# Optimization experiments

Measured on AMD Instinct MI355X. Metric: run time of the kernel, lower is better.

Reference implementation:

```python
import jax, jax.numpy as jnp
import numpy as np

B, N, D, K = 32, 4096, 128, 512
NPB = 2048          # unique tail nodes per batch (>= K so topk branch is taken)
M = B * NPB         # total unique tail nodes
E = B * N           # total edges
NUM_ENT = 10000


def setup_inputs() -> dict:
    key = jax.random.key(0)
    ks = jax.random.split(key, 18)
    f = lambda k, s: jax.random.normal(k, s, dtype=jnp.float32)
    inp = {
        "q_head": f(ks[0], (B, D)),
        "q_rel": f(ks[1], (B, D)),
        "q_time": f(ks[2], (B, D)),
        "r_neighbor": f(ks[3], (B, N, D)),
        "t_neighbor": f(ks[4], (B, N, D)),
        "time_neighbor": f(ks[5], (B, N, D)),
        "hidden": f(ks[6], (E, D)),
        "tail_emd": jnp.zeros((M, D), jnp.float32),  # scatter out-buffer
    }
    # tail_index: each edge of batch b scatters into that batch's node slab
    local = jax.random.randint(ks[7], (B, N), 0, NPB)
    inp["tail_index"] = (local + jnp.arange(B)[:, None] * NPB).reshape(E).astype(jnp.int32)
    # tail_nodes: [M,3] = (batch id, tail entity, time)
    batch_col = jnp.repeat(jnp.arange(B), NPB)
    tail_col = jax.random.randint(ks[8], (M,), 0, NUM_ENT)
    time_col = jax.random.randint(ks[9], (M,), 0, 365)
    inp["tail_nodes"] = jnp.stack([batch_col, tail_col, time_col], axis=-1).astype(jnp.int32)
    # linear-layer params (torch nn.Linear-style scaling)
    s3, s1 = 1.0 / np.sqrt(3 * D), 1.0 / np.sqrt(D)
    inp["W_q"] = f(ks[10], (3 * D, D)) * s3
    inp["b_q"] = jnp.zeros((D,), jnp.float32)
    inp["W_a"] = f(ks[11], (3 * D, D)) * s3
    inp["b_a"] = jnp.zeros((D,), jnp.float32)
    inp["W_att"] = f(ks[12], (3 * D, 1)) * s3
    inp["b_att"] = jnp.zeros((1,), jnp.float32)
    inp["W_rule"] = f(ks[13], (D, 1)) * s1
    inp["b_rule"] = jnp.zeros((1,), jnp.float32)
    inp["W_out"] = f(ks[14], (D, D)) * s1
    inp["b_out"] = jnp.zeros((D,), jnp.float32)
    return inp


def reference(q_head, q_rel, q_time, r_neighbor, t_neighbor, time_neighbor,
              hidden, tail_emd, tail_index, tail_nodes,
              W_q, b_q, W_a, b_a, W_att, b_att, W_rule, b_rule, W_out, b_out):
    # act = identity (module default). reduce = 'sum'.
    # raw message per edge: [E, D]
    message = (q_head[:, None, :] + r_neighbor + time_neighbor).reshape(E, D)
    # query / neighbor projections
    query = jnp.concatenate([q_head, q_rel, q_time], axis=-1) @ W_q + b_q      # [B, D]
    neigh = jnp.concatenate([r_neighbor, t_neighbor, time_neighbor], -1) @ W_a + b_a  # [B, N, D]
    q = query[:, None, :]
    qa = jnp.concatenate([q * neigh, q - neigh, q + neigh], axis=-1)           # [B, N, 3D]
    att1 = jax.nn.sigmoid(qa @ W_att + b_att).reshape(E, 1)
    att2 = jax.nn.sigmoid(hidden @ W_rule + b_rule)                            # [E, 1]
    att = (att1 + att2) * 0.5
    msg = att * message
    # scatter-sum aggregation over unique tail nodes
    seg = lambda v: jax.ops.segment_sum(v, tail_index, num_segments=M)
    tail_agg = tail_emd + seg(msg)            # scatter(..., out=tail_emd)
    new_hidden = seg(hidden)                  # [M, D]
    agg_att = seg(att[:, 0])                  # [M]
    # per-batch top-k over aggregated attention (each batch has NPB >= K nodes)
    nodes_batch = tail_nodes[:, 0]
    scores = jnp.where(nodes_batch[None, :] == jnp.arange(B)[:, None],
                       agg_att[None, :], -jnp.inf)                             # [B, M]
    _, idx = jax.lax.top_k(scores, K)                                          # [B, K] global node ids
    new_nodes = jnp.stack([tail_nodes[:, 1][idx], tail_nodes[:, 2][idx]], -1)  # [B, K, 2]
    emd = tail_agg[idx]                                                        # [B, K, D]
    hid = new_hidden[idx]                                                      # [B, K, D]
    out_emd = emd @ W_out + b_out                                              # act=identity
    return new_nodes, out_emd, hid
```

## Files before the change

### kernel.cpp

```cpp
#include <hip/hip_runtime.h>
#include <math.h>

#define B 32
#define N 4096
#define D 128
#define KTOP 512
#define NPB 2048
#define MSEG (B * NPB)
#define E (B * N)
#define MAXC 32
#define K7ROWS 16

__global__ __launch_bounds__(384) void k0_precompute(
    const float* __restrict__ qh, const float* __restrict__ qr,
    const float* __restrict__ qt, const float* __restrict__ Wq,
    const float* __restrict__ bq, const float* __restrict__ Wa,
    const float* __restrict__ ba, const float* __restrict__ Watt,
    const float* __restrict__ batt, float* __restrict__ vf,
    float* __restrict__ c2f, int* __restrict__ counts,
    double* __restrict__ aggd) {
  int b = blockIdx.x;
  int tid = threadIdx.x;
  {
    int t = b * 384 + tid;
    float4 z = make_float4(0.f, 0.f, 0.f, 0.f);
    float4* cz = (float4*)counts;
    float4* az = (float4*)aggd;
    for (int i = t; i < 16384; i += 12288) cz[i] = z;
    for (int i = t; i < 32768; i += 12288) az[i] = z;
  }
  int d = tid & 127;
  int g = tid >> 7;
  __shared__ double part[3][128];
  __shared__ double u[128];
  __shared__ double red[128];
  const float* xs = (g == 0 ? qh : (g == 1 ? qr : qt)) + b * 128;
  const float* Wg = Wq + g * 128 * 128;
  double a0 = 0, a1 = 0, a2 = 0, a3 = 0;
#pragma unroll 4
  for (int i = 0; i < 128; i += 4) {
    a0 += (double)xs[i] * (double)Wg[i * 128 + d];
    a1 += (double)xs[i + 1] * (double)Wg[(i + 1) * 128 + d];
    a2 += (double)xs[i + 2] * (double)Wg[(i + 2) * 128 + d];
    a3 += (double)xs[i + 3] * (double)Wg[(i + 3) * 128 + d];
  }
  part[g][d] = (a0 + a1) + (a2 + a3);
  __syncthreads();
  if (g == 0) {
    double acc = (double)bq[d] + part[0][d] + part[1][d] + part[2][d];
    double w1 = (double)Watt[d], w2 = (double)Watt[128 + d],
           w3 = (double)Watt[256 + d];
    double ud = acc * w1 - w2 + w3;
    u[d] = ud;
    red[d] = acc * (w2 + w3) + (double)ba[d] * ud;
  }
  __syncthreads();
  for (int s = 64; s > 0; s >>= 1) {
    if (tid < s) red[tid] += red[tid + s];
    __syncthreads();
  }
  if (tid == 0) c2f[b] = (float)(red[0] + (double)batt[0]);
  {
    double v0 = 0, v1 = 0, v2 = 0, v3 = 0;
    const float* Wr = Wa + tid * 128;
#pragma unroll 4
    for (int dd = 0; dd < 128; dd += 4) {
      v0 += (double)Wr[dd] * u[dd];
      v1 += (double)Wr[dd + 1] * u[dd + 1];
      v2 += (double)Wr[dd + 2] * u[dd + 2];
      v3 += (double)Wr[dd + 3] * u[dd + 3];
    }
    vf[b * 384 + tid] = (float)((v0 + v1) + (v2 + v3));
  }
}

__global__ __launch_bounds__(256, 8) void k1_att(
    const float* __restrict__ r, const float* __restrict__ t,
    const float* __restrict__ tm, const float* __restrict__ hidden,
    const float* __restrict__ Wrule, const float* __restrict__ brule,
    const float* __restrict__ vf, const float* __restrict__ c2f,
    const int* __restrict__ tidx, float* __restrict__ attw,
    double* __restrict__ aggd, int* __restrict__ counts,
    unsigned short* __restrict__ lists) {
  int tid = threadIdx.x;
  int h = tid >> 5;
  int l = tid & 31;
  int blk = blockIdx.x;
  int b = blk >> 5;
  const float4* vb = (const float4*)(vf + b * 384);
  float4 v0 = vb[l];
  float4 v1 = vb[32 + l];
  float4 v2 = vb[64 + l];
  float4 wr = ((const float4*)Wrule)[l];
  float c2 = c2f[b];
  float br = brule[0];
  unsigned lo = (unsigned)(l * 4);
  for (int pass = 0; pass < 2; ++pass) {
    int base = blk * 128 + pass * 64;
    int myseg = 0;
    if (l < 8) myseg = tidx[base + l * 8 + h];
    float mya = 0.f;
    float4 ra[2], ta[2], ma[2], ha[2];
    {
      unsigned eo = ((unsigned)(base + h) << 7) + lo;
      ra[0] = *(const float4*)(r + eo);
      ta[0] = *(const float4*)(t + eo);
      ma[0] = *(const float4*)(tm + eo);
      ha[0] = *(const float4*)(hidden + eo);
    }
#pragma unroll
    for (int i = 0; i < 8; ++i) {
      const int cur = i & 1;
      if (i < 7) {
        const int nxt = cur ^ 1;
        unsigned eo = ((unsigned)(base + (i + 1) * 8 + h) << 7) + lo;
        ra[nxt] = *(const float4*)(r + eo);
        ta[nxt] = *(const float4*)(t + eo);
        ma[nxt] = *(const float4*)(tm + eo);
        ha[nxt] = *(const float4*)(hidden + eo);
      }
      float4 A = ra[cur], T = ta[cur], M = ma[cur], H = ha[cur];
      float p1 = A.x * v0.x + A.y * v0.y + A.z * v0.z + A.w * v0.w;
      p1 += T.x * v1.x + T.y * v1.y + T.z * v1.z + T.w * v1.w;
      p1 += M.x * v2.x + M.y * v2.y + M.z * v2.z + M.w * v2.w;
      float p2 = H.x * wr.x + H.y * wr.y + H.z * wr.z + H.w * wr.w;
#pragma unroll
      for (int off = 16; off > 0; off >>= 1) {
        p1 += __shfl_xor(p1, off);
        p2 += __shfl_xor(p2, off);
      }
      if (l == i) {
        float a1 = 1.0f / (1.0f + expf(-(p1 + c2)));
        float a2 = 1.0f / (1.0f + expf(-(p2 + br)));
        mya = 0.5f * (a1 + a2);
      }
    }
    if (l < 8) {
      int e = base + l * 8 + h;
      attw[e] = mya;
      atomicAdd(&aggd[myseg], (double)mya);
      int pos = atomicAdd(&counts[myseg], 1);
      if (pos < MAXC)
        lists[(unsigned)myseg * MAXC + pos] = (unsigned short)(e & 4095);
    }
  }
}

__global__ __launch_bounds__(256) void k6_topk(
    const double* __restrict__ aggd, const int* __restrict__ tail_nodes,
    float* __restrict__ out_nodes, int* __restrict__ idxw) {
  __shared__ double sv[2048];
  int b = blockIdx.x >> 3;
  int chunk = blockIdx.x & 7;
  int tid = threadIdx.x;
  for (int s = tid; s < 2048; s += 256) sv[s] = aggd[b * 2048 + s];
  __syncthreads();
  int i = chunk * 256 + tid;
  double vi = sv[i];
  int rank = 0;
#pragma unroll 8
  for (int j = 0; j < 2048; ++j) {
    double vj = sv[j];
    rank += (vj > vi) || (vj == vi && j < i);
  }
  if (rank < KTOP) {
    int gm = b * 2048 + i;
    int p = b * KTOP + rank;
    out_nodes[p * 2 + 0] = (float)tail_nodes[gm * 3 + 1];
    out_nodes[p * 2 + 1] = (float)tail_nodes[gm * 3 + 2];
    idxw[p] = gm;
  }
}

__global__ __launch_bounds__(256) void k7_out(
    const float* __restrict__ tail_emd, const float* __restrict__ r,
    const float* __restrict__ tm, const float* __restrict__ hidden,
    const float* __restrict__ qh, const float* __restrict__ attw,
    const int* __restrict__ counts, const unsigned short* __restrict__ lists,
    const float* __restrict__ Wout, const float* __restrict__ bout,
    const int* __restrict__ idxw, float* __restrict__ out_emd,
    float* __restrict__ out_hid) {
  __shared__ float es[K7ROWS][128];
  int tid = threadIdx.x;
  int sub = tid >> 7, d = tid & 127;
  int base = blockIdx.x * K7ROWS;
  int mrow[8], crow[8];
#pragma unroll
  for (int jj = 0; jj < 8; ++jj) mrow[jj] = idxw[base + jj * 2 + sub];
#pragma unroll
  for (int jj = 0; jj < 8; ++jj) crow[jj] = counts[mrow[jj]];
  uint2 el[8];
#pragma unroll
  for (int jj = 0; jj < 8; ++jj)
    el[jj] = *(const uint2*)(lists + (size_t)mrow[jj] * MAXC);
#pragma unroll
  for (int jj = 0; jj < 8; ++jj) {
    int m = mrow[jj];
    int bb = m >> 11;
    unsigned ebase = (unsigned)bb << 12;
    int cnt = crow[jj] > MAXC ? MAXC : crow[jj];
    float accT = tail_emd[(size_t)m * 128 + d];
    float accH = 0.f;
    float qhd = qh[bb * 128 + d];
    unsigned e0 = ebase | (el[jj].x & 0xFFFFu);
    unsigned e1 = ebase | (el[jj].x >> 16);
    unsigned e2 = ebase | (el[jj].y & 0xFFFFu);
    unsigned e3 = ebase | (el[jj].y >> 16);
    float m0 = cnt > 0 ? 1.f : 0.f;
    float m1 = cnt > 1 ? 1.f : 0.f;
    float m2 = cnt > 2 ? 1.f : 0.f;
    float m3 = cnt > 3 ? 1.f : 0.f;
    float a0 = attw[e0], a1 = attw[e1], a2 = attw[e2], a3 = attw[e3];
    unsigned o0 = (e0 << 7) + d, o1 = (e1 << 7) + d;
    unsigned o2 = (e2 << 7) + d, o3 = (e3 << 7) + d;
    float r0 = r[o0], r1 = r[o1], r2 = r[o2], r3 = r[o3];
    float t0 = tm[o0], t1 = tm[o1], t2 = tm[o2], t3 = tm[o3];
    float h0 = hidden[o0], h1 = hidden[o1], h2 = hidden[o2], h3 = hidden[o3];
    accT += m0 * a0 * (qhd + r0 + t0);
    accT += m1 * a1 * (qhd + r1 + t1);
    accT += m2 * a2 * (qhd + r2 + t2);
    accT += m3 * a3 * (qhd + r3 + t3);
    accH += m0 * h0 + m1 * h1 + m2 * h2 + m3 * h3;
    for (int k = 4; k < cnt; ++k) {
      unsigned e = ebase | lists[(size_t)m * MAXC + k];
      float a = attw[e];
      unsigned eo = (e << 7) + d;
      accT += a * (qhd + r[eo] + tm[eo]);
      accH += hidden[eo];
    }
    es[jj * 2 + sub][d] = accT;
    out_hid[(size_t)(base + jj * 2 + sub) * 128 + d] = accH;
  }
  __syncthreads();
  int cg = tid & 31;
  int rg = tid >> 5;
  float4 bo = *(const float4*)(bout + cg * 4);
  float acc0x = bo.x, acc0y = bo.y, acc0z = bo.z, acc0w = bo.w;
  float acc1x = bo.x, acc1y = bo.y, acc1z = bo.z, acc1w = bo.w;
#pragma unroll 4
  for (int i = 0; i < 128; ++i) {
    float4 w = *(const float4*)(Wout + i * 128 + cg * 4);
    float e0 = es[rg * 2 + 0][i];
    float e1 = es[rg * 2 + 1][i];
    acc0x += e0 * w.x; acc0y += e0 * w.y; acc0z += e0 * w.z; acc0w += e0 * w.w;
    acc1x += e1 * w.x; acc1y += e1 * w.y; acc1z += e1 * w.z; acc1w += e1 * w.w;
  }
  size_t r0o = (size_t)(base + rg * 2) * 128 + cg * 4;
  *(float4*)(out_emd + r0o) = make_float4(acc0x, acc0y, acc0z, acc0w);
  *(float4*)(out_emd + r0o + 128) = make_float4(acc1x, acc1y, acc1z, acc1w);
}

extern "C" void kernel_launch(void* const* d_in, const int* in_sizes, int n_in,
                              void* d_out, int out_size, void* d_ws,
                              size_t ws_size, hipStream_t stream) {
  const float* q_head = (const float*)d_in[0];
  const float* q_rel = (const float*)d_in[1];
  const float* q_time = (const float*)d_in[2];
  const float* r_nb = (const float*)d_in[3];
  const float* t_nb = (const float*)d_in[4];
  const float* tm_nb = (const float*)d_in[5];
  const float* hidden = (const float*)d_in[6];
  const float* tail_emd = (const float*)d_in[7];
  const int* tail_index = (const int*)d_in[8];
  const int* tail_nodes = (const int*)d_in[9];
  const float* W_q = (const float*)d_in[10];
  const float* b_q = (const float*)d_in[11];
  const float* W_a = (const float*)d_in[12];
  const float* b_a = (const float*)d_in[13];
  const float* W_att = (const float*)d_in[14];
  const float* b_att = (const float*)d_in[15];
  const float* W_rule = (const float*)d_in[16];
  const float* b_rule = (const float*)d_in[17];
  const float* W_out = (const float*)d_in[18];
  const float* b_out = (const float*)d_in[19];

  char* ws = (char*)d_ws;
  float* vf = (float*)(ws + 0);
  float* c2f = (float*)(ws + 49152);
  float* attw = (float*)(ws + 49280);
  int* counts = (int*)(ws + 573568);
  double* aggd = (double*)(ws + 835712);
  unsigned short* lists = (unsigned short*)(ws + 1360000);
  int* idxw = (int*)(ws + 5554304);

  float* out_nodes = (float*)d_out;
  float* out_emd = (float*)d_out + (size_t)B * KTOP * 2;
  float* out_hid = out_emd + (size_t)B * KTOP * 128;

  k0_precompute<<<B, 384, 0, stream>>>(q_head, q_rel, q_time, W_q, b_q, W_a,
                                       b_a, W_att, b_att, vf, c2f, counts,
                                       aggd);
  k1_att<<<E / 128, 256, 0, stream>>>(r_nb, t_nb, tm_nb, hidden, W_rule,
                                      b_rule, vf, c2f, tail_index, attw, aggd,
                                      counts, lists);
  k6_topk<<<B * 8, 256, 0, stream>>>(aggd, tail_nodes, out_nodes, idxw);
  k7_out<<<(B * KTOP) / K7ROWS, 256, 0, stream>>>(tail_emd, r_nb, tm_nb,
                                                  hidden, q_head, attw, counts,
                                                  lists, W_out, b_out, idxw,
                                                  out_emd, out_hid);
}
```

Baseline: 424.9 us.

## Replace global atomic scatter and brute-force topk with per-batch LDS counting-sort kernel

Strips the global double atomics and the capped per-segment edge lists out of the attention kernel. A new per-batch kernel accumulates attention into LDS with fixed-point integer atomics and builds CSR offsets with a counting sort over edges. It then selects the top-k with a histogram bucket on the high bits followed by exact ranking only within the boundary bucket. This removes the global atomic contention, the O(N^2) rank loop and the MAXC truncation, at the cost of a low-parallelism 32-block kernel and fixed-point rounding of the aggregated scores.

```diff
diff --git a/kernel.cpp b/kernel.cpp
--- a/kernel.cpp
+++ b/kernel.cpp
@@ -8,7 +8,6 @@
 #define NPB 2048
 #define MSEG (B * NPB)
 #define E (B * N)
-#define MAXC 32
 #define K7ROWS 16
 
 __global__ __launch_bounds__(384) void k0_precompute(
@@ -17,18 +16,9 @@
     const float* __restrict__ bq, const float* __restrict__ Wa,
     const float* __restrict__ ba, const float* __restrict__ Watt,
     const float* __restrict__ batt, float* __restrict__ vf,
-    float* __restrict__ c2f, int* __restrict__ counts,
-    double* __restrict__ aggd) {
+    float* __restrict__ c2f) {
   int b = blockIdx.x;
   int tid = threadIdx.x;
-  {
-    int t = b * 384 + tid;
-    float4 z = make_float4(0.f, 0.f, 0.f, 0.f);
-    float4* cz = (float4*)counts;
-    float4* az = (float4*)aggd;
-    for (int i = t; i < 16384; i += 12288) cz[i] = z;
-    for (int i = t; i < 32768; i += 12288) az[i] = z;
-  }
   int d = tid & 127;
   int g = tid >> 7;
   __shared__ double part[3][128];
@@ -79,14 +69,12 @@
     const float* __restrict__ tm, const float* __restrict__ hidden,
     const float* __restrict__ Wrule, const float* __restrict__ brule,
     const float* __restrict__ vf, const float* __restrict__ c2f,
-    const int* __restrict__ tidx, float* __restrict__ attw,
-    double* __restrict__ aggd, int* __restrict__ counts,
-    unsigned short* __restrict__ lists) {
+    float* __restrict__ attw) {
   int tid = threadIdx.x;
   int h = tid >> 5;
   int l = tid & 31;
-  int blk = blockIdx.x;
-  int b = blk >> 5;
+  int base = blockIdx.x * 64;
+  int b = base >> 12;
   const float4* vb = (const float4*)(vf + b * 384);
   float4 v0 = vb[l];
   float4 v1 = vb[32 + l];
@@ -94,81 +82,159 @@
   float4 wr = ((const float4*)Wrule)[l];
   float c2 = c2f[b];
   float br = brule[0];
+  float mya = 0.f;
   unsigned lo = (unsigned)(l * 4);
-  for (int pass = 0; pass < 2; ++pass) {
-    int base = blk * 128 + pass * 64;
-    int myseg = 0;
-    if (l < 8) myseg = tidx[base + l * 8 + h];
-    float mya = 0.f;
-    float4 ra[2], ta[2], ma[2], ha[2];
-    {
-      unsigned eo = ((unsigned)(base + h) << 7) + lo;
-      ra[0] = *(const float4*)(r + eo);
-      ta[0] = *(const float4*)(t + eo);
-      ma[0] = *(const float4*)(tm + eo);
-      ha[0] = *(const float4*)(hidden + eo);
-    }
-#pragma unroll
-    for (int i = 0; i < 8; ++i) {
-      const int cur = i & 1;
-      if (i < 7) {
-        const int nxt = cur ^ 1;
-        unsigned eo = ((unsigned)(base + (i + 1) * 8 + h) << 7) + lo;
-        ra[nxt] = *(const float4*)(r + eo);
-        ta[nxt] = *(const float4*)(t + eo);
-        ma[nxt] = *(const float4*)(tm + eo);
-        ha[nxt] = *(const float4*)(hidden + eo);
-      }
-      float4 A = ra[cur], T = ta[cur], M = ma[cur], H = ha[cur];
-      float p1 = A.x * v0.x + A.y * v0.y + A.z * v0.z + A.w * v0.w;
-      p1 += T.x * v1.x + T.y * v1.y + T.z * v1.z + T.w * v1.w;
-      p1 += M.x * v2.x + M.y * v2.y + M.z * v2.z + M.w * v2.w;
-      float p2 = H.x * wr.x + H.y * wr.y + H.z * wr.z + H.w * wr.w;
-#pragma unroll
-      for (int off = 16; off > 0; off >>= 1) {
-        p1 += __shfl_xor(p1, off);
-        p2 += __shfl_xor(p2, off);
-      }
-      if (l == i) {
-        float a1 = 1.0f / (1.0f + expf(-(p1 + c2)));
-        float a2 = 1.0f / (1.0f + expf(-(p2 + br)));
-        mya = 0.5f * (a1 + a2);
-      }
-    }
-    if (l < 8) {
-      int e = base + l * 8 + h;
-      attw[e] = mya;
-      atomicAdd(&aggd[myseg], (double)mya);
-      int pos = atomicAdd(&counts[myseg], 1);
-      if (pos < MAXC)
-        lists[(unsigned)myseg * MAXC + pos] = (unsigned short)(e & 4095);
-    }
-  }
-}
-
-__global__ __launch_bounds__(256) void k6_topk(
-    const double* __restrict__ aggd, const int* __restrict__ tail_nodes,
-    float* __restrict__ out_nodes, int* __restrict__ idxw) {
-  __shared__ double sv[2048];
-  int b = blockIdx.x >> 3;
-  int chunk = blockIdx.x & 7;
+  float4 ra[2], ta[2], ma[2], ha[2];
+  {
+    unsigned eo = ((unsigned)(base + h) << 7) + lo;
+    ra[0] = *(const float4*)(r + eo);
+    ta[0] = *(const float4*)(t + eo);
+    ma[0] = *(const float4*)(tm + eo);
+    ha[0] = *(const float4*)(hidden + eo);
+  }
+#pragma unroll
+  for (int i = 0; i < 8; ++i) {
+    const int cur = i & 1;
+    if (i < 7) {
+      const int nxt = cur ^ 1;
+      unsigned eo = ((unsigned)(base + (i + 1) * 8 + h) << 7) + lo;
+      ra[nxt] = *(const float4*)(r + eo);
+      ta[nxt] = *(const float4*)(t + eo);
+      ma[nxt] = *(const float4*)(tm + eo);
+      ha[nxt] = *(const float4*)(hidden + eo);
+    }
+    float4 A = ra[cur], T = ta[cur], M = ma[cur], H = ha[cur];
+    float p1 = A.x * v0.x + A.y * v0.y + A.z * v0.z + A.w * v0.w;
+    p1 += T.x * v1.x + T.y * v1.y + T.z * v1.z + T.w * v1.w;
+    p1 += M.x * v2.x + M.y * v2.y + M.z * v2.z + M.w * v2.w;
+    float p2 = H.x * wr.x + H.y * wr.y + H.z * wr.z + H.w * wr.w;
+#pragma unroll
+    for (int off = 16; off > 0; off >>= 1) {
+      p1 += __shfl_xor(p1, off);
+      p2 += __shfl_xor(p2, off);
+    }
+    if (l == i) {
+      float a1 = 1.0f / (1.0f + expf(-(p1 + c2)));
+      float a2 = 1.0f / (1.0f + expf(-(p2 + br)));
+      mya = 0.5f * (a1 + a2);
+    }
+  }
+  if (l < 8) attw[base + l * 8 + h] = mya;
+}
+
+__global__ __launch_bounds__(512) void k2_agg(
+    const float* __restrict__ attw, const int* __restrict__ tidx,
+    const int* __restrict__ tail_nodes, unsigned* __restrict__ offp,
+    unsigned short* __restrict__ packed, float* __restrict__ out_nodes,
+    int* __restrict__ idxw) {
+  __shared__ unsigned long long aggu[2048];
+  __shared__ unsigned cnt[2048];
+  __shared__ unsigned off[2048];
+  __shared__ unsigned partial[512];
+  __shared__ unsigned hist[512];
+  __shared__ unsigned hsuf[513];
+  __shared__ unsigned hstart[512];
+  __shared__ unsigned bcur[512];
+  __shared__ unsigned short sorted[2048];
+  int b = blockIdx.x;
   int tid = threadIdx.x;
-  for (int s = tid; s < 2048; s += 256) sv[s] = aggd[b * 2048 + s];
-  __syncthreads();
-  int i = chunk * 256 + tid;
-  double vi = sv[i];
-  int rank = 0;
-#pragma unroll 8
-  for (int j = 0; j < 2048; ++j) {
-    double vj = sv[j];
-    rank += (vj > vi) || (vj == vi && j < i);
-  }
-  if (rank < KTOP) {
-    int gm = b * 2048 + i;
-    int p = b * KTOP + rank;
-    out_nodes[p * 2 + 0] = (float)tail_nodes[gm * 3 + 1];
-    out_nodes[p * 2 + 1] = (float)tail_nodes[gm * 3 + 2];
-    idxw[p] = gm;
+  for (int i = tid; i < 2048; i += 512) { aggu[i] = 0ull; cnt[i] = 0u; }
+  if (tid < 512) hist[tid] = 0u;
+  __syncthreads();
+  int ebase = b * 4096;
+  int locseg[8];
+  float av[8];
+#pragma unroll
+  for (int k = 0; k < 8; ++k) {
+    int e = ebase + tid + k * 512;
+    locseg[k] = tidx[e] & 2047;
+    av[k] = attw[e];
+  }
+#pragma unroll
+  for (int k = 0; k < 8; ++k) {
+    unsigned long long q =
+        (unsigned long long)((double)av[k] * 144115188075855872.0);
+    atomicAdd(&aggu[locseg[k]], q);
+    atomicAdd(&cnt[locseg[k]], 1u);
+  }
+  __syncthreads();
+  {
+    unsigned c0 = cnt[tid * 4], c1 = cnt[tid * 4 + 1];
+    unsigned c2v = cnt[tid * 4 + 2], c3 = cnt[tid * 4 + 3];
+    unsigned s = c0 + c1 + c2v + c3;
+    partial[tid] = s;
+    __syncthreads();
+    for (int st = 1; st < 512; st <<= 1) {
+      unsigned x = partial[tid];
+      unsigned y = (tid >= st) ? partial[tid - st] : 0u;
+      __syncthreads();
+      partial[tid] = x + y;
+      __syncthreads();
+    }
+    unsigned basep = partial[tid] - s;
+    off[tid * 4] = basep;
+    off[tid * 4 + 1] = basep + c0;
+    off[tid * 4 + 2] = basep + c0 + c1;
+    off[tid * 4 + 3] = basep + c0 + c1 + c2v;
+  }
+  __syncthreads();
+  for (int i = tid; i < 2048; i += 512)
+    offp[b * 2048 + i] = (unsigned)(b * 4096) + off[i];
+  if (b == B - 1 && tid == 0) offp[MSEG] = E;
+  for (int i = tid; i < 2048; i += 512)
+    atomicAdd(&hist[(unsigned)(aggu[i] >> 54)], 1u);
+  __syncthreads();
+  for (int i = tid; i < 2048; i += 512) cnt[i] = off[i];
+  __syncthreads();
+#pragma unroll
+  for (int k = 0; k < 8; ++k) {
+    unsigned pos = atomicAdd(&cnt[locseg[k]], 1u);
+    packed[b * 4096 + pos] = (unsigned short)(tid + k * 512);
+  }
+  {
+    partial[tid] = hist[tid];
+    __syncthreads();
+    for (int st = 1; st < 512; st <<= 1) {
+      unsigned x = partial[tid];
+      unsigned y = (tid >= st) ? partial[tid - st] : 0u;
+      __syncthreads();
+      partial[tid] = x + y;
+      __syncthreads();
+    }
+    unsigned fex = partial[tid] - hist[tid];
+    hstart[tid] = fex;
+    hsuf[tid] = 2048u - fex;
+    if (tid == 0) hsuf[512] = 0u;
+    bcur[tid] = fex;
+    __syncthreads();
+  }
+  for (int i = tid; i < 2048; i += 512) {
+    unsigned bkt = (unsigned)(aggu[i] >> 54);
+    unsigned p = atomicAdd(&bcur[bkt], 1u);
+    sorted[p] = (unsigned short)i;
+  }
+  __syncthreads();
+  for (int c = 0; c < 4; ++c) {
+    int i = c * 512 + tid;
+    unsigned long long vi = aggu[i];
+    unsigned bkt = (unsigned)(vi >> 54);
+    unsigned above = hsuf[bkt + 1];
+    if (above >= KTOP) continue;
+    unsigned rank = above;
+    unsigned s0 = hstart[bkt];
+    unsigned s1 = s0 + (hsuf[bkt] - hsuf[bkt + 1]);
+    for (unsigned k = s0; k < s1; ++k) {
+      int j = sorted[k];
+      unsigned long long vj = aggu[j];
+      rank += (vj > vi) || (vj == vi && j < i);
+    }
+    if (rank < KTOP) {
+      int gm = b * 2048 + i;
+      int p = b * KTOP + (int)rank;
+      out_nodes[p * 2 + 0] = (float)tail_nodes[gm * 3 + 1];
+      out_nodes[p * 2 + 1] = (float)tail_nodes[gm * 3 + 2];
+      idxw[p] = gm;
+    }
   }
 }
 
@@ -176,7 +242,7 @@
     const float* __restrict__ tail_emd, const float* __restrict__ r,
     const float* __restrict__ tm, const float* __restrict__ hidden,
     const float* __restrict__ qh, const float* __restrict__ attw,
-    const int* __restrict__ counts, const unsigned short* __restrict__ lists,
+    const unsigned* __restrict__ offp, const unsigned short* __restrict__ packed,
     const float* __restrict__ Wout, const float* __restrict__ bout,
     const int* __restrict__ idxw, float* __restrict__ out_emd,
     float* __restrict__ out_hid) {
@@ -184,28 +250,35 @@
   int tid = threadIdx.x;
   int sub = tid >> 7, d = tid & 127;
   int base = blockIdx.x * K7ROWS;
-  int mrow[8], crow[8];
+  int mrow[8];
+  unsigned o0r[8], cntr[8];
 #pragma unroll
   for (int jj = 0; jj < 8; ++jj) mrow[jj] = idxw[base + jj * 2 + sub];
 #pragma unroll
-  for (int jj = 0; jj < 8; ++jj) crow[jj] = counts[mrow[jj]];
-  uint2 el[8];
+  for (int jj = 0; jj < 8; ++jj) {
+    unsigned o0 = offp[mrow[jj]];
+    unsigned o1 = offp[mrow[jj] + 1];
+    o0r[jj] = o0;
+    cntr[jj] = o1 - o0;
+  }
+  unsigned short e4[8][4];
 #pragma unroll
   for (int jj = 0; jj < 8; ++jj)
-    el[jj] = *(const uint2*)(lists + (size_t)mrow[jj] * MAXC);
+#pragma unroll
+    for (int k = 0; k < 4; ++k) e4[jj][k] = packed[o0r[jj] + k];
 #pragma unroll
   for (int jj = 0; jj < 8; ++jj) {
     int m = mrow[jj];
     int bb = m >> 11;
     unsigned ebase = (unsigned)bb << 12;
-    int cnt = crow[jj] > MAXC ? MAXC : crow[jj];
+    int cnt = (int)cntr[jj];
     float accT = tail_emd[(size_t)m * 128 + d];
     float accH = 0.f;
     float qhd = qh[bb * 128 + d];
-    unsigned e0 = ebase | (el[jj].x & 0xFFFFu);
-    unsigned e1 = ebase | (el[jj].x >> 16);
-    unsigned e2 = ebase | (el[jj].y & 0xFFFFu);
-    unsigned e3 = ebase | (el[jj].y >> 16);
+    unsigned e0 = ebase | (e4[jj][0] & 4095u);
+    unsigned e1 = ebase | (e4[jj][1] & 4095u);
+    unsigned e2 = ebase | (e4[jj][2] & 4095u);
+    unsigned e3 = ebase | (e4[jj][3] & 4095u);
     float m0 = cnt > 0 ? 1.f : 0.f;
     float m1 = cnt > 1 ? 1.f : 0.f;
     float m2 = cnt > 2 ? 1.f : 0.f;
@@ -222,7 +295,7 @@
     accT += m3 * a3 * (qhd + r3 + t3);
     accH += m0 * h0 + m1 * h1 + m2 * h2 + m3 * h3;
     for (int k = 4; k < cnt; ++k) {
-      unsigned e = ebase | lists[(size_t)m * MAXC + k];
+      unsigned e = ebase | (packed[o0r[jj] + k] & 4095u);
       float a = attw[e];
       unsigned eo = (e << 7) + d;
       accT += a * (qhd + r[eo] + tm[eo]);
@@ -278,24 +351,22 @@
   float* vf = (float*)(ws + 0);
   float* c2f = (float*)(ws + 49152);
   float* attw = (float*)(ws + 49280);
-  int* counts = (int*)(ws + 573568);
-  double* aggd = (double*)(ws + 835712);
-  unsigned short* lists = (unsigned short*)(ws + 1360000);
-  int* idxw = (int*)(ws + 5554304);
+  unsigned* offp = (unsigned*)(ws + 573568);
+  unsigned short* packed = (unsigned short*)(ws + 835776);
+  int* idxw = (int*)(ws + 1097984);
 
   float* out_nodes = (float*)d_out;
   float* out_emd = (float*)d_out + (size_t)B * KTOP * 2;
   float* out_hid = out_emd + (size_t)B * KTOP * 128;
 
   k0_precompute<<<B, 384, 0, stream>>>(q_head, q_rel, q_time, W_q, b_q, W_a,
-                                       b_a, W_att, b_att, vf, c2f, counts,
-                                       aggd);
-  k1_att<<<E / 128, 256, 0, stream>>>(r_nb, t_nb, tm_nb, hidden, W_rule,
-                                      b_rule, vf, c2f, tail_index, attw, aggd,
-                                      counts, lists);
-  k6_topk<<<B * 8, 256, 0, stream>>>(aggd, tail_nodes, out_nodes, idxw);
+                                       b_a, W_att, b_att, vf, c2f);
+  k1_att<<<E / 64, 256, 0, stream>>>(r_nb, t_nb, tm_nb, hidden, W_rule, b_rule,
+                                     vf, c2f, attw);
+  k2_agg<<<B, 512, 0, stream>>>(attw, tail_index, tail_nodes, offp, packed,
+                                out_nodes, idxw);
   k7_out<<<(B * KTOP) / K7ROWS, 256, 0, stream>>>(tail_emd, r_nb, tm_nb,
-                                                  hidden, q_head, attw, counts,
-                                                  lists, W_out, b_out, idxw,
+                                                  hidden, q_head, attw, offp,
+                                                  packed, W_out, b_out, idxw,
                                                   out_emd, out_hid);
 }
```

New measurement: 435.2 us. 2.4% more time.
